# Kernel optimization log

Measured on AMD Instinct MI355X. Metric: run time of the kernel, lower is better.

Reference implementation:

```python
import jax, jax.numpy as jnp
import numpy as np

NUM_EMBEDDINGS = 512
EMBEDDING_DIM = 128
COMMITMENT = 0.25
DECAY = 0.99
EPS = 1e-05


def setup_inputs() -> dict:
    key = jax.random.key(0)
    k1, k2 = jax.random.split(key)
    z = jax.random.normal(k1, (32, EMBEDDING_DIM, 64, 64), dtype=jnp.float32)
    embedding = jax.random.normal(k2, (EMBEDDING_DIM, NUM_EMBEDDINGS), dtype=jnp.float32)
    cluster_size = jnp.zeros((NUM_EMBEDDINGS,), dtype=jnp.float32)
    embed_avg = embedding  # buffer initialized as a clone of embedding
    return {"z": z, "embedding": embedding, "cluster_size": cluster_size, "embed_avg": embed_avg}


def reference(z, embedding, cluster_size, embed_avg):
    sg = jax.lax.stop_gradient
    D, K = embedding.shape
    B, C, H, W = z.shape
    z_perm = jnp.transpose(z, (0, 2, 3, 1))          # [B,H,W,D]
    flat_z = z_perm.reshape(-1, D)                    # [N,D]

    distances = ((flat_z ** 2).sum(1, keepdims=True)
                 - 2.0 * (flat_z @ embedding)
                 + (embedding ** 2).sum(0)[None, :])  # [N,K]
    idx = jnp.argmin(distances, axis=1)               # [N]

    # gather codes (equivalent to one-hot @ embedding.T, without materializing one-hot)
    quantized = jnp.take(embedding.T, idx, axis=0).reshape(z_perm.shape)  # [B,H,W,D]
    quantized = jnp.transpose(quantized, (0, 3, 1, 2))                    # [B,D,H,W]

    # EMA codebook update (training branch)
    enc_sum = jax.ops.segment_sum(jnp.ones_like(idx, dtype=flat_z.dtype), idx, num_segments=K)  # [K]
    embed_sum = jax.ops.segment_sum(flat_z, idx, num_segments=K).T                              # [D,K]
    new_cluster_size = cluster_size * DECAY + (1.0 - DECAY) * enc_sum
    new_embed_avg = embed_avg * DECAY + (1.0 - DECAY) * embed_sum
    n = jnp.maximum(new_cluster_size.sum(), 1e-05)
    cs = (new_cluster_size + EPS) / (n + K * EPS) * n
    new_embedding = new_embed_avg / cs[None, :]

    e_latent_loss = jnp.mean((sg(quantized) - z) ** 2)
    q_latent_loss = jnp.mean((quantized - sg(z)) ** 2)
    loss = q_latent_loss + COMMITMENT * e_latent_loss

    quantized_out = z + sg(quantized - z)             # straight-through
    encoding_indices = idx.reshape(B, H, W)
    return (quantized_out, loss, encoding_indices, new_embedding, new_cluster_size, new_embed_avg)
```

## Files before the change

### kernel.cpp

```cpp
#include <hip/hip_runtime.h>
#include <hip/hip_bf16.h>
#include <float.h>

typedef _Float16 f16;
typedef __attribute__((ext_vector_type(8))) _Float16 half8;
typedef __attribute__((ext_vector_type(4))) float floatx4;

#define DIM   128
#define HW    4096
#define NPOS  131072
#define K     512
#define ZSTRIDE_B 524288

#define Q_OFF     0
#define LOSS_OFF  16777216
#define IDX_OFF   16777217
#define NEMB_OFF  16908289
#define NCS_OFF   16973825
#define NEA_OFF   16974337

#define WS_E2    0
#define WS_ENC   512
#define WS_ESUM  1024
#define WS_EHI   1024
#define WS_ELO   33792
#define WS_LOSS  66560
#define WS_NN    66561

#define XST 136

__global__ __launch_bounds__(256) void k_prep(const float* __restrict__ emb,
                                              f16* __restrict__ ehiP,
                                              f16* __restrict__ eloP,
                                              float* __restrict__ e2) {
    int lin = blockIdx.x * 256 + threadIdx.x;
    int d = lin >> 9, k = lin & 511;
    float v = emb[lin];
    atomicAdd(&e2[k], v * v);
    f16 h = (f16)v;
    f16 l = (f16)(v - (float)h);
    int g = k >> 4, r = k & 15;
    int dc = d >> 5, w = d & 31, quad = w >> 3, j = w & 7;
    int idx = (g * 4 + dc) * 512 + quad * 128 + r * 8 + j;
    ehiP[idx] = h;
    eloP[idx] = l;
}

__global__ __launch_bounds__(256) void k_assign(const float* __restrict__ z,
                                                const f16* __restrict__ ehiP,
                                                const f16* __restrict__ eloP,
                                                const float* __restrict__ e2,
                                                float* __restrict__ out) {
    __shared__ f16 xs_h[64 * XST];
    __shared__ f16 xs_l[64 * XST];
    __shared__ float wbD[256];
    __shared__ int   wbI[256];

    const int tid  = threadIdx.x;
    const int lane = tid & 63;
    const int wv   = tid >> 6;
    const int n0   = blockIdx.x * 64;
    const int b    = n0 >> 12;
    const int hw0  = n0 & 4095;
    const float* zb = z + b * ZSTRIDE_B + hw0;
    const int l15  = lane & 15;
    const int quad = lane >> 4;

    #pragma unroll
    for (int it = 0; it < 16; ++it) {
        int lin = tid + it * 256;
        int i  = lin & 63;
        int dp = lin >> 6;
        float v0 = zb[(2 * dp) * HW + i];
        float v1 = zb[(2 * dp + 1) * HW + i];
        f16 h0 = (f16)v0; f16 l0 = (f16)(v0 - (float)h0);
        f16 h1 = (f16)v1; f16 l1 = (f16)(v1 - (float)h1);
        union { f16 h[2]; unsigned int u; } ph, pl;
        ph.h[0] = h0; ph.h[1] = h1;
        pl.h[0] = l0; pl.h[1] = l1;
        *(unsigned int*)&xs_h[i * XST + 2 * dp] = ph.u;
        *(unsigned int*)&xs_l[i * XST + 2 * dp] = pl.u;
    }
    __syncthreads();

    float bestD[4][4];
    int   bestI[4][4];
    #pragma unroll
    for (int t = 0; t < 4; ++t)
        #pragma unroll
        for (int r = 0; r < 4; ++r) { bestD[t][r] = FLT_MAX; bestI[t][r] = 0x7fffffff; }

    const half8* gh = (const half8*)ehiP;
    const half8* gl = (const half8*)eloP;

    for (int nc = 0; nc < 2; ++nc) {
        floatx4 acc[4][4];
        #pragma unroll
        for (int t = 0; t < 4; ++t)
            #pragma unroll
            for (int nt = 0; nt < 4; ++nt) acc[t][nt] = (floatx4){0.f, 0.f, 0.f, 0.f};

        for (int dc = 0; dc < 4; ++dc) {
            half8 ah[4], al[4];
            #pragma unroll
            for (int t = 0; t < 4; ++t) {
                int off = (t * 16 + l15) * XST + dc * 32 + quad * 8;
                ah[t] = *(const half8*)&xs_h[off];
                al[t] = *(const half8*)&xs_l[off];
            }
            #pragma unroll
            for (int nt = 0; nt < 4; ++nt) {
                int bi = ((nc * 16 + wv * 4 + nt) * 4 + dc) * 64 + lane;
                half8 bh = gh[bi];
                half8 bl = gl[bi];
                #pragma unroll
                for (int t = 0; t < 4; ++t) {
                    acc[t][nt] = __builtin_amdgcn_mfma_f32_16x16x32_f16(ah[t], bh, acc[t][nt], 0, 0, 0);
                    acc[t][nt] = __builtin_amdgcn_mfma_f32_16x16x32_f16(al[t], bh, acc[t][nt], 0, 0, 0);
                    acc[t][nt] = __builtin_amdgcn_mfma_f32_16x16x32_f16(ah[t], bl, acc[t][nt], 0, 0, 0);
                }
            }
        }
        #pragma unroll
        for (int nt = 0; nt < 4; ++nt) {
            int c = nc * 256 + wv * 64 + nt * 16 + l15;
            float ee = e2[c];
            #pragma unroll
            for (int t = 0; t < 4; ++t)
                #pragma unroll
                for (int r = 0; r < 4; ++r) {
                    float s = fmaf(-2.f, acc[t][nt][r], ee);
                    if (s < bestD[t][r]) { bestD[t][r] = s; bestI[t][r] = c; }
                }
        }
    }

    #pragma unroll
    for (int mask = 1; mask <= 8; mask <<= 1) {
        #pragma unroll
        for (int t = 0; t < 4; ++t)
            #pragma unroll
            for (int r = 0; r < 4; ++r) {
                float od = __shfl_xor(bestD[t][r], mask, 64);
                int   oi = __shfl_xor(bestI[t][r], mask, 64);
                if (od < bestD[t][r] || (od == bestD[t][r] && oi < bestI[t][r])) {
                    bestD[t][r] = od; bestI[t][r] = oi;
                }
            }
    }
    if (l15 == 0) {
        #pragma unroll
        for (int t = 0; t < 4; ++t)
            #pragma unroll
            for (int r = 0; r < 4; ++r) {
                int m = t * 16 + quad * 4 + r;
                wbD[wv * 64 + m] = bestD[t][r];
                wbI[wv * 64 + m] = bestI[t][r];
            }
    }
    __syncthreads();
    if (tid < 64) {
        float bd = wbD[tid]; int bi = wbI[tid];
        #pragma unroll
        for (int w = 1; w < 4; ++w) {
            float od = wbD[w * 64 + tid]; int oi = wbI[w * 64 + tid];
            if (od < bd || (od == bd && oi < bi)) { bd = od; bi = oi; }
        }
        out[IDX_OFF + n0 + tid] = (float)bi;
    }
}

#define DC 8
__global__ __launch_bounds__(256) void k_ema2(const float* __restrict__ z,
                                              const float* __restrict__ emb,
                                              float* __restrict__ out,
                                              float* __restrict__ enc,
                                              float* __restrict__ esum,
                                              float* __restrict__ lossAcc) {
    __shared__ float acc[DC][K];
    __shared__ float embs[DC][K];
    __shared__ float cnt[K];
    __shared__ float wred[4];

    const int tid = threadIdx.x;
    const int lane = tid & 63;
    const int wv = tid >> 6;
    const int dchunk = blockIdx.x & 15;
    const int b      = blockIdx.x >> 4;
    const int d0 = dchunk * DC;
    const bool doCnt = (dchunk == 0);

    for (int i = tid; i < DC * K; i += 256) {
        ((float*)acc)[i] = 0.f;
        ((float*)embs)[i] = emb[d0 * K + i];
    }
    if (doCnt) for (int i = tid; i < K; i += 256) cnt[i] = 0.f;
    __syncthreads();

    const float* zb  = z + b * ZSTRIDE_B;
    const float* idp = out + IDX_OFF + b * HW;
    float* qb = out + Q_OFF + b * ZSTRIDE_B;
    float lsum = 0.f;

    for (int t = 0; t < HW; t += 1024) {
        const int p = t + 4 * tid;
        int k0 = (int)idp[p + 0];
        int k1 = (int)idp[p + 1];
        int k2 = (int)idp[p + 2];
        int k3 = (int)idp[p + 3];
        if (doCnt) {
            atomicAdd(&cnt[k0], 1.f); atomicAdd(&cnt[k1], 1.f);
            atomicAdd(&cnt[k2], 1.f); atomicAdd(&cnt[k3], 1.f);
        }
        #pragma unroll
        for (int d = 0; d < DC; ++d) {
            float4 zv = *(const float4*)(zb + (d0 + d) * HW + p);
            atomicAdd(&acc[d][k0], zv.x);
            atomicAdd(&acc[d][k1], zv.y);
            atomicAdd(&acc[d][k2], zv.z);
            atomicAdd(&acc[d][k3], zv.w);
            float4 qv;
            qv.x = embs[d][k0]; qv.y = embs[d][k1];
            qv.z = embs[d][k2]; qv.w = embs[d][k3];
            *(float4*)(qb + (d0 + d) * HW + p) = qv;
            float dx = qv.x - zv.x; lsum = fmaf(dx, dx, lsum);
            float dy = qv.y - zv.y; lsum = fmaf(dy, dy, lsum);
            float dz2 = qv.z - zv.z; lsum = fmaf(dz2, dz2, lsum);
            float dw = qv.w - zv.w; lsum = fmaf(dw, dw, lsum);
        }
    }

    #pragma unroll
    for (int m = 32; m >= 1; m >>= 1) lsum += __shfl_xor(lsum, m, 64);
    if (lane == 0) wred[wv] = lsum;
    __syncthreads();
    if (tid == 0) atomicAdd(lossAcc, wred[0] + wred[1] + wred[2] + wred[3]);

    for (int i = tid; i < DC * K; i += 256) {
        int d = i >> 9, k = i & 511;
        atomicAdd(&esum[(d0 + d) * K + k], acc[d][k]);
    }
    if (doCnt) for (int i = tid; i < K; i += 256) atomicAdd(&enc[i], cnt[i]);
}

__global__ __launch_bounds__(512) void k_final(const float* __restrict__ enc,
                                               const float* __restrict__ cs_in,
                                               const float* __restrict__ lossAcc,
                                               float* __restrict__ out,
                                               float* __restrict__ nnOut) {
    __shared__ float red[512];
    int k = threadIdx.x;
    float ncs = fmaf(cs_in[k], 0.99f, 0.01f * enc[k]);
    red[k] = ncs;
    out[NCS_OFF + k] = ncs;
    __syncthreads();
    for (int s = 256; s > 0; s >>= 1) {
        if (k < s) red[k] += red[k + s];
        __syncthreads();
    }
    if (k == 0) {
        nnOut[0] = fmaxf(red[0], 1e-5f);
        out[LOSS_OFF] = lossAcc[0] * 1.25f / 16777216.0f;
    }
}

__global__ __launch_bounds__(512) void k_final2(const float* __restrict__ esum,
                                                const float* __restrict__ eavg_in,
                                                const float* __restrict__ nnIn,
                                                float* __restrict__ out) {
    int d = blockIdx.x;
    int k = threadIdx.x;
    float nn = nnIn[0];
    float ncs = out[NCS_OFF + k];
    float cs = (ncs + 1e-5f) / (nn + (float)K * 1e-5f) * nn;
    float ea = fmaf(eavg_in[d * K + k], 0.99f, 0.01f * esum[d * K + k]);
    out[NEA_OFF + d * K + k] = ea;
    out[NEMB_OFF + d * K + k] = ea / cs;
}

extern "C" void kernel_launch(void* const* d_in, const int* in_sizes, int n_in,
                              void* d_out, int out_size, void* d_ws, size_t ws_size,
                              hipStream_t stream) {
    const float* z     = (const float*)d_in[0];
    const float* emb   = (const float*)d_in[1];
    const float* cs_in = (const float*)d_in[2];
    const float* eavg  = (const float*)d_in[3];
    float* out = (float*)d_out;
    float* wsF = (float*)d_ws;

    hipMemsetAsync(wsF + WS_E2, 0, 1024 * sizeof(float), stream);
    hipMemsetAsync(wsF + WS_LOSS, 0, sizeof(float), stream);

    k_prep<<<256, 256, 0, stream>>>(emb, (f16*)(wsF + WS_EHI), (f16*)(wsF + WS_ELO),
                                    wsF + WS_E2);
    k_assign<<<NPOS / 64, 256, 0, stream>>>(z,
                                            (const f16*)(wsF + WS_EHI),
                                            (const f16*)(wsF + WS_ELO),
                                            wsF + WS_E2, out);
    hipMemsetAsync(wsF + WS_ESUM, 0, 65536 * sizeof(float), stream);
    k_ema2<<<512, 256, 0, stream>>>(z, emb, out, wsF + WS_ENC, wsF + WS_ESUM,
                                    wsF + WS_LOSS);
    k_final<<<1, 512, 0, stream>>>(wsF + WS_ENC, cs_in, wsF + WS_LOSS,
                                   out, wsF + WS_NN);
    k_final2<<<128, 512, 0, stream>>>(wsF + WS_ESUM, eavg, wsF + WS_NN, out);
}
```

Measured before the change: 330.6 us.

## Cut assign register pressure, batch z loads, split EMA over two halves

```diff
diff --git a/kernel.cpp b/kernel.cpp
--- a/kernel.cpp
+++ b/kernel.cpp
@@ -46,11 +46,11 @@
     eloP[idx] = l;
 }
 
-__global__ __launch_bounds__(256) void k_assign(const float* __restrict__ z,
-                                                const f16* __restrict__ ehiP,
-                                                const f16* __restrict__ eloP,
-                                                const float* __restrict__ e2,
-                                                float* __restrict__ out) {
+__global__ __launch_bounds__(256, 2) void k_assign(const float* __restrict__ z,
+                                                   const f16* __restrict__ ehiP,
+                                                   const f16* __restrict__ eloP,
+                                                   const float* __restrict__ e2,
+                                                   float* __restrict__ out) {
     __shared__ f16 xs_h[64 * XST];
     __shared__ f16 xs_l[64 * XST];
     __shared__ float wbD[256];
@@ -66,13 +66,21 @@
     const int l15  = lane & 15;
     const int quad = lane >> 4;
 
+    float sv0[16], sv1[16];
     #pragma unroll
     for (int it = 0; it < 16; ++it) {
         int lin = tid + it * 256;
         int i  = lin & 63;
         int dp = lin >> 6;
-        float v0 = zb[(2 * dp) * HW + i];
-        float v1 = zb[(2 * dp + 1) * HW + i];
+        sv0[it] = zb[(2 * dp) * HW + i];
+        sv1[it] = zb[(2 * dp + 1) * HW + i];
+    }
+    #pragma unroll
+    for (int it = 0; it < 16; ++it) {
+        int lin = tid + it * 256;
+        int i  = lin & 63;
+        int dp = lin >> 6;
+        float v0 = sv0[it], v1 = sv1[it];
         f16 h0 = (f16)v0; f16 l0 = (f16)(v0 - (float)h0);
         f16 h1 = (f16)v1; f16 l1 = (f16)(v1 - (float)h1);
         union { f16 h[2]; unsigned int u; } ph, pl;
@@ -93,12 +101,12 @@
     const half8* gh = (const half8*)ehiP;
     const half8* gl = (const half8*)eloP;
 
-    for (int nc = 0; nc < 2; ++nc) {
-        floatx4 acc[4][4];
+    for (int cc = 0; cc < 4; ++cc) {
+        floatx4 acc[4][2];
         #pragma unroll
         for (int t = 0; t < 4; ++t)
             #pragma unroll
-            for (int nt = 0; nt < 4; ++nt) acc[t][nt] = (floatx4){0.f, 0.f, 0.f, 0.f};
+            for (int nt = 0; nt < 2; ++nt) acc[t][nt] = (floatx4){0.f, 0.f, 0.f, 0.f};
 
         for (int dc = 0; dc < 4; ++dc) {
             half8 ah[4], al[4];
@@ -109,8 +117,9 @@
                 al[t] = *(const half8*)&xs_l[off];
             }
             #pragma unroll
-            for (int nt = 0; nt < 4; ++nt) {
-                int bi = ((nc * 16 + wv * 4 + nt) * 4 + dc) * 64 + lane;
+            for (int nt = 0; nt < 2; ++nt) {
+                int g  = cc * 8 + wv * 2 + nt;
+                int bi = (g * 4 + dc) * 64 + lane;
                 half8 bh = gh[bi];
                 half8 bl = gl[bi];
                 #pragma unroll
@@ -122,8 +131,8 @@
             }
         }
         #pragma unroll
-        for (int nt = 0; nt < 4; ++nt) {
-            int c = nc * 256 + wv * 64 + nt * 16 + l15;
+        for (int nt = 0; nt < 2; ++nt) {
+            int c = cc * 128 + wv * 32 + nt * 16 + l15;
             float ee = e2[c];
             #pragma unroll
             for (int t = 0; t < 4; ++t)
@@ -185,8 +194,9 @@
     const int tid = threadIdx.x;
     const int lane = tid & 63;
     const int wv = tid >> 6;
-    const int dchunk = blockIdx.x & 15;
-    const int b      = blockIdx.x >> 4;
+    const int half   = blockIdx.x & 1;
+    const int dchunk = (blockIdx.x >> 1) & 15;
+    const int b      = blockIdx.x >> 5;
     const int d0 = dchunk * DC;
     const bool doCnt = (dchunk == 0);
 
@@ -202,12 +212,14 @@
     float* qb = out + Q_OFF + b * ZSTRIDE_B;
     float lsum = 0.f;
 
-    for (int t = 0; t < HW; t += 1024) {
+    const int p0 = half * 2048;
+    for (int t = p0; t < p0 + 2048; t += 1024) {
         const int p = t + 4 * tid;
-        int k0 = (int)idp[p + 0];
-        int k1 = (int)idp[p + 1];
-        int k2 = (int)idp[p + 2];
-        int k3 = (int)idp[p + 3];
+        float4 iv = *(const float4*)(idp + p);
+        int k0 = (int)iv.x;
+        int k1 = (int)iv.y;
+        int k2 = (int)iv.z;
+        int k3 = (int)iv.w;
         if (doCnt) {
             atomicAdd(&cnt[k0], 1.f); atomicAdd(&cnt[k1], 1.f);
             atomicAdd(&cnt[k2], 1.f); atomicAdd(&cnt[k3], 1.f);
@@ -298,8 +310,8 @@
                                             (const f16*)(wsF + WS_ELO),
                                             wsF + WS_E2, out);
     hipMemsetAsync(wsF + WS_ESUM, 0, 65536 * sizeof(float), stream);
-    k_ema2<<<512, 256, 0, stream>>>(z, emb, out, wsF + WS_ENC, wsF + WS_ESUM,
-                                    wsF + WS_LOSS);
+    k_ema2<<<1024, 256, 0, stream>>>(z, emb, out, wsF + WS_ENC, wsF + WS_ESUM,
+                                     wsF + WS_LOSS);
     k_final<<<1, 512, 0, stream>>>(wsF + WS_ENC, cs_in, wsF + WS_LOSS,
                                    out, wsF + WS_NN);
     k_final2<<<128, 512, 0, stream>>>(wsF + WS_ESUM, eavg, wsF + WS_NN, out);
```

Measured after the change: 291.1 us. -12.0%, faster.
